# Performance work log

Hardware: AMD Instinct MI355X
Metric: run time of the kernel (lower is better)

## Reference

```python
import jax, jax.numpy as jnp
import numpy as np

# Static problem sizes (match input_specs): B graphs of NPG nodes each.
B = 64        # number of graphs in the batch
NPG = 1024    # nodes per graph
N = B * NPG   # total nodes
F = 64        # node feature dim
H = 128       # MLP hidden/output dim
K = 16        # knn neighbors (loop=False)


def setup_inputs() -> dict:
    key = jax.random.key(0)
    k1, k2, k3 = jax.random.split(key, 3)
    x = jax.random.normal(k1, (N, F), dtype=jnp.float32)
    batch = jnp.repeat(jnp.arange(B, dtype=jnp.int32), NPG)  # sorted graph ids
    W1 = jax.random.normal(k2, (2 * F, H), dtype=jnp.float32) / np.float32(np.sqrt(2 * F))
    b1 = jnp.zeros((H,), dtype=jnp.float32)
    W2 = jax.random.normal(k3, (H, H), dtype=jnp.float32) / np.float32(np.sqrt(H))
    b2 = jnp.zeros((H,), dtype=jnp.float32)
    return {"x": x, "batch": batch, "W1": W1, "b1": b1, "W2": W2, "b2": b2}


def _knn_edge_index(x):
    """PyG-style knn_graph (flow='source_to_target', loop=False) per graph.
    Returns (row, col) = edge_index[0], edge_index[1] where row = neighbor
    (source) node, col = center (target) node; each center has exactly K edges.
    Assumes batch ids are contiguous blocks of NPG nodes (as in setup_inputs)."""
    xb = x.reshape(B, NPG, F)
    sq = jnp.sum(xb * xb, axis=-1)                                   # [B, n]
    d = sq[:, :, None] + sq[:, None, :] - 2.0 * jnp.einsum('bnf,bmf->bnm', xb, xb)
    d = d + jnp.eye(NPG, dtype=d.dtype) * jnp.float32(1e10)          # no self loops
    _, nbr = jax.lax.top_k(-d, K)                                    # [B, n, K] local neighbor ids
    offs = (jnp.arange(B, dtype=jnp.int32) * NPG)[:, None, None]
    row = (nbr.astype(jnp.int32) + offs).reshape(-1)                 # neighbors (edge_index[0])
    centers = jnp.arange(N, dtype=jnp.int32).reshape(B, NPG, 1)
    col = jnp.broadcast_to(centers, (B, NPG, K)).reshape(-1)         # centers  (edge_index[1])
    return row, col


def reference(x, batch, W1, b1, W2, b2):
    # edge_index = knn_graph(x, k, batch, loop=False); row, col = edge_index
    row, col = _knn_edge_index(x)
    x_center = x[row]                                   # [E, F] gather
    x_neighbor = x[col]                                 # [E, F] gather
    ef = jnp.concatenate([x_center, x_neighbor - x_center], axis=-1)  # [E, 2F]
    # nn_module: Linear -> ReLU -> Linear -> ReLU
    h = jax.nn.relu(ef @ W1 + b1)
    h = jax.nn.relu(h @ W2 + b2)                        # [E, H]
    # manual scatter-mean onto row (index_add + bincount.clamp(min=1))
    node_features = jax.ops.segment_sum(h, row, num_segments=N)
    counts = jax.ops.segment_sum(jnp.ones((row.shape[0],), dtype=x.dtype), row, num_segments=N)
    counts = jnp.maximum(counts, 1.0)
    return node_features / counts[:, None]
```

## Files before the change

### kernel.cpp

```cpp
#include <hip/hip_runtime.h>

typedef __attribute__((ext_vector_type(4))) float f32x4;
typedef __attribute__((ext_vector_type(4))) unsigned int u32x4;
typedef __attribute__((ext_vector_type(8))) short s16x8;
typedef __attribute__((ext_vector_type(8))) _Float16 f16x8;

#define N_NODES 65536
#define GNPG 1024
#define FDIM 64
#define HDIM 128
#define KNN 16
#define JT 64
#define DSTR 68
#define SCAND 20
#define STKC 6
#define NEDGE (N_NODES * KNN)
#define NT (NEDGE / 64)

__global__ void prep_node_k(const float* __restrict__ x, float* __restrict__ sq,
                            double* __restrict__ sq64, _Float16* __restrict__ xf,
                            const float* __restrict__ W2, _Float16* __restrict__ w2f,
                            const float* __restrict__ W1, _Float16* __restrict__ w1cf) {
  if (blockIdx.x >= 1024) {
    int tid = threadIdx.x;
    if (blockIdx.x == 1024) {
      for (int idx = tid; idx < 8 * 4 * 64 * 8; idx += 256) {
        int j = idx & 7, l = (idx >> 3) & 63, ks = (idx >> 9) & 3, ct = idx >> 11;
        int k = 8 * (l >> 4) + j + 32 * ks, col = ct * 16 + (l & 15);
        w2f[idx] = (_Float16)W2[k * 128 + col];
      }
    } else {
      for (int idx = tid; idx < 16 * 2 * 64 * 8; idx += 256) {
        int j = idx & 7, l = (idx >> 3) & 63, ks = (idx >> 9) & 1, ct = idx >> 10;
        int k = 8 * (l >> 4) + j + 32 * ks, col = ct * 16 + (l & 15);
        float v = (col < 128) ? (W1[k * 128 + col] - W1[(k + 64) * 128 + col])
                              : W1[(k + 64) * 128 + (col - 128)];
        w1cf[idx] = (_Float16)v;
      }
    }
    return;
  }
  int t = blockIdx.x * 256 + threadIdx.x;
  int n = t >> 2, q = t & 3;
  const f32x4* xp = (const f32x4*)(x + (size_t)n * FDIM + q * 16);
  double s = 0;
  f16x8 h0, h1;
#pragma unroll
  for (int c8 = 0; c8 < 2; ++c8) {
    f32x4 a = xp[2 * c8], b = xp[2 * c8 + 1];
    f16x8 h;
#pragma unroll
    for (int e = 0; e < 4; ++e) {
      h[e] = (_Float16)a[e];
      h[4 + e] = (_Float16)b[e];
      s = fma((double)a[e], (double)a[e], s);
      s = fma((double)b[e], (double)b[e], s);
    }
    if (c8 == 0) h0 = h; else h1 = h;
  }
  *(f16x8*)(xf + (size_t)n * FDIM + q * 16) = h0;
  *(f16x8*)(xf + (size_t)n * FDIM + q * 16 + 8) = h1;
  s += __shfl_xor(s, 1);
  s += __shfl_xor(s, 2);
  if (q == 0) { sq64[n] = s; sq[n] = (float)s; }
}

__global__ __launch_bounds__(256) void prep_pq_k(const _Float16* __restrict__ xf,
                                                 const _Float16* __restrict__ w1cf,
                                                 const float* __restrict__ b1,
                                                 _Float16* __restrict__ PQ16) {
  __shared__ __attribute__((aligned(16))) _Float16 wcL[16384];
  int tid = threadIdx.x, lane = tid & 63, wave = tid >> 6;
  for (int i = tid; i < 2048; i += 256)
    *(f16x8*)(wcL + i * 8) = *(const f16x8*)(w1cf + i * 8);
  int rbase = blockIdx.x * 128 + wave * 32;
  f16x8 af[2][2];
#pragma unroll
  for (int rt = 0; rt < 2; ++rt)
#pragma unroll
    for (int ks = 0; ks < 2; ++ks) {
      size_t off = (size_t)(rbase + rt * 16 + (lane & 15)) * FDIM + (lane >> 4) * 8 + 32 * ks;
      af[rt][ks] = *(const f16x8*)(xf + off);
    }
  __syncthreads();
  f32x4 acc[2][16];
#pragma unroll
  for (int rt = 0; rt < 2; ++rt)
#pragma unroll
    for (int ct = 0; ct < 16; ++ct) acc[rt][ct] = (f32x4){0.f, 0.f, 0.f, 0.f};
#pragma unroll
  for (int ks = 0; ks < 2; ++ks)
#pragma unroll
    for (int ct = 0; ct < 16; ++ct) {
      f16x8 b = *(const f16x8*)(wcL + ((ct * 2 + ks) * 64 + lane) * 8);
#pragma unroll
      for (int rt = 0; rt < 2; ++rt)
        acc[rt][ct] = __builtin_amdgcn_mfma_f32_16x16x32_f16(af[rt][ks], b, acc[rt][ct], 0, 0, 0);
    }
  float b1r[16];
#pragma unroll
  for (int ct = 0; ct < 16; ++ct)
    b1r[ct] = (ct >= 8) ? b1[(ct - 8) * 16 + (lane & 15)] : 0.f;
#pragma unroll
  for (int rt = 0; rt < 2; ++rt)
#pragma unroll
    for (int ct = 0; ct < 16; ++ct) {
      int col = ct * 16 + (lane & 15);
#pragma unroll
      for (int r = 0; r < 4; ++r) {
        int row = rbase + rt * 16 + (lane >> 4) * 4 + r;
        PQ16[(size_t)row * 256 + col] = (_Float16)(acc[rt][ct][r] + b1r[ct]);
      }
    }
}

__global__ __launch_bounds__(256) void knn1_k(const _Float16* __restrict__ xf,
                                              const float* __restrict__ sq,
                                              unsigned short* __restrict__ candi) {
  __shared__ float sq_l[GNPG];
  __shared__ __attribute__((aligned(16))) _Float16 bfL[512 * 8];
  __shared__ __attribute__((aligned(16))) unsigned keyL[128 * DSTR];
  __shared__ __attribute__((aligned(16))) unsigned stk[STKC * 256];
  int tid = threadIdx.x, lane = tid & 63, wave = tid >> 6;
  int g = blockIdx.x >> 3;
  int rb = (blockIdx.x & 7) * 128;
  const _Float16* xfg = xf + (size_t)g * GNPG * FDIM;
  for (int i = tid; i < GNPG; i += 256) sq_l[i] = sq[g * GNPG + i] + 0.5f;
  f16x8 af[2][2];
#pragma unroll
  for (int rt = 0; rt < 2; ++rt)
#pragma unroll
    for (int ks = 0; ks < 2; ++ks) {
      size_t off = (size_t)(rb + wave * 32 + rt * 16 + (lane & 15)) * FDIM + (lane >> 4) * 8 + 32 * ks;
      af[rt][ks] = *(const f16x8*)(xfg + off);
    }
  unsigned dl[SCAND];
#pragma unroll
  for (int q = 0; q < SCAND; ++q) dl[q] = 0xFFFFFFFFu;
  int c = tid >> 1, sub = tid & 1;
  int sp = 0;
  for (int jt = 0; jt < GNPG / JT; ++jt) {
#pragma unroll
    for (int s2 = tid; s2 < 512; s2 += 256) {
      int ct = s2 >> 7, ks = (s2 >> 6) & 1, l = s2 & 63;
      size_t goff = (size_t)(jt * JT + ct * 16 + (l & 15)) * FDIM + (l >> 4) * 8 + 32 * ks;
      *(f16x8*)(bfL + s2 * 8) = *(const f16x8*)(xfg + goff);
    }
    __syncthreads();
    f32x4 acc[2][4];
#pragma unroll
    for (int rt = 0; rt < 2; ++rt)
#pragma unroll
      for (int ct = 0; ct < 4; ++ct) acc[rt][ct] = (f32x4){0.f, 0.f, 0.f, 0.f};
#pragma unroll
    for (int ks = 0; ks < 2; ++ks)
#pragma unroll
      for (int ct = 0; ct < 4; ++ct) {
        f16x8 bfr = *(const f16x8*)(bfL + ((ct * 2 + ks) * 64 + lane) * 8);
#pragma unroll
        for (int rt = 0; rt < 2; ++rt)
          acc[rt][ct] = __builtin_amdgcn_mfma_f32_16x16x32_f16(af[rt][ks], bfr, acc[rt][ct], 0, 0, 0);
      }
#pragma unroll
    for (int rt = 0; rt < 2; ++rt)
#pragma unroll
      for (int ct = 0; ct < 4; ++ct) {
        int coltl = ct * 16 + (lane & 15);
        int jlg = jt * JT + coltl;
        float sqj = sq_l[jlg];
#pragma unroll
        for (int r = 0; r < 4; ++r) {
          int row = wave * 32 + rt * 16 + (lane >> 4) * 4 + r;
          float d = sq_l[rb + row] + sqj - 2.f * acc[rt][ct][r];
          unsigned key = (__float_as_uint(d) & 0xFFFFFC00u) | (unsigned)jlg;
          if (rb + row == jlg) key = 0xFFFFFFFFu;
          keyL[row * DSTR + coltl] = key;
        }
      }
    __syncthreads();
    const unsigned* kp = keyL + c * DSTR + sub * 32;
    u32x4 vv[8];
#pragma unroll
    for (int i = 0; i < 8; ++i) vv[i] = *(const u32x4*)(kp + i * 4);
#pragma unroll
    for (int i = 0; i < 8; ++i) {
      if (__any(sp > STKC - 4)) {
        while (__any(sp > 0)) {
          if (sp > 0) {
            --sp;
            unsigned k = stk[sp * 256 + tid];
            if (k < dl[SCAND - 1]) {
              dl[SCAND - 1] = k;
#pragma unroll
              for (int p = SCAND - 1; p >= 1; --p) {
                unsigned mn = min(dl[p - 1], dl[p]);
                unsigned mx = max(dl[p - 1], dl[p]);
                dl[p - 1] = mn; dl[p] = mx;
              }
            }
          }
        }
      }
#pragma unroll
      for (int e = 0; e < 4; ++e) {
        stk[sp * 256 + tid] = vv[i][e];
        sp += (vv[i][e] < dl[SCAND - 1]) ? 1 : 0;
      }
    }
  }
  while (__any(sp > 0)) {
    if (sp > 0) {
      --sp;
      unsigned k = stk[sp * 256 + tid];
      if (k < dl[SCAND - 1]) {
        dl[SCAND - 1] = k;
#pragma unroll
        for (int p = SCAND - 1; p >= 1; --p) {
          unsigned mn = min(dl[p - 1], dl[p]);
          unsigned mx = max(dl[p - 1], dl[p]);
          dl[p - 1] = mn; dl[p] = mx;
        }
      }
    }
  }
  int nglob = g * GNPG + rb + c;
  unsigned short* ii = candi + (size_t)nglob * (2 * SCAND) + sub * SCAND;
#pragma unroll
  for (int q = 0; q < SCAND; ++q) ii[q] = (unsigned short)(dl[q] & 1023u);
}

__global__ __launch_bounds__(256) void knn2_k(const float* __restrict__ x,
                                              const double* __restrict__ sq64,
                                              const unsigned short* __restrict__ candi,
                                              int* __restrict__ nbr, int* __restrict__ counts) {
  __shared__ double md[2][128][17];
  __shared__ unsigned short mi[2][128][17];
  int tid = threadIdx.x, c_local = tid >> 1, sub = tid & 1;
  int n = blockIdx.x * 128 + c_local;
  int gbase = n & ~(GNPG - 1);
  f32x4 xi[16];
  const f32x4* xp = (const f32x4*)(x + (size_t)n * FDIM);
#pragma unroll
  for (int f = 0; f < 16; ++f) xi[f] = xp[f];
  double sq64i = sq64[n];
  double dl[KNN]; int il[KNN];
#pragma unroll
  for (int q = 0; q < KNN; ++q) { dl[q] = 1.0e300; il[q] = 0x7FFFFFFF; }
  const unsigned short* ii = candi + (size_t)n * (2 * SCAND) + sub * SCAND;
#pragma unroll 1
  for (int t = 0; t < SCAND; ++t) {
    int jl = ii[t];
    int j = gbase + jl;
    const f32x4* xj = (const f32x4*)(x + (size_t)j * FDIM);
    double t0 = 0, t1 = 0, t2 = 0, t3 = 0;
#pragma unroll
    for (int f = 0; f < 16; ++f) {
      f32x4 a = xi[f], b = xj[f];
      t0 = fma((double)a[0], (double)b[0], t0);
      t1 = fma((double)a[1], (double)b[1], t1);
      t2 = fma((double)a[2], (double)b[2], t2);
      t3 = fma((double)a[3], (double)b[3], t3);
    }
    double d = sq64i + sq64[j] - 2.0 * ((t0 + t1) + (t2 + t3));
    bool ins = (d < dl[KNN - 1]) || (d == dl[KNN - 1] && jl < il[KNN - 1]);
    if (ins) {
      dl[KNN - 1] = d; il[KNN - 1] = jl;
#pragma unroll
      for (int p = KNN - 1; p >= 1; --p) {
        double a0 = dl[p - 1], a1 = dl[p];
        int b0 = il[p - 1], b1v = il[p];
        bool cc = (a1 < a0) || (a1 == a0 && b1v < b0);
        dl[p - 1] = cc ? a1 : a0; dl[p] = cc ? a0 : a1;
        il[p - 1] = cc ? b1v : b0; il[p] = cc ? b0 : b1v;
      }
    }
  }
#pragma unroll
  for (int q = 0; q < KNN; ++q) {
    md[sub][c_local][q] = dl[q];
    mi[sub][c_local][q] = (unsigned short)il[q];
  }
  __syncthreads();
  if (sub == 0) {
    int pa = 0, pb = 0;
    for (int q = 0; q < KNN; ++q) {
      double da = md[0][c_local][pa]; int ia = mi[0][c_local][pa];
      double db = md[1][c_local][pb]; int ib = mi[1][c_local][pb];
      bool tb = (db < da) || (db == da && ib < ia);
      int iw = tb ? ib : ia;
      pa += !tb; pb += tb;
      int gidx = gbase + iw;
      nbr[(size_t)n * KNN + q] = gidx;
      atomicAdd(&counts[gidx], 1);
    }
  }
}

__global__ void scan_k(const int* __restrict__ counts, int* __restrict__ cursor) {
  __shared__ int wsum[16];
  int t = threadIdx.x;
  int base = t * 64;
  const int4* cp = (const int4*)(counts + base);
  int s = 0;
#pragma unroll
  for (int i = 0; i < 16; ++i) { int4 v = cp[i]; s += v.x + v.y + v.z + v.w; }
  int lane = t & 63, wv = t >> 6;
  int pre = s;
#pragma unroll
  for (int ofs = 1; ofs < 64; ofs <<= 1) {
    int o = __shfl_up(pre, ofs);
    if (lane >= ofs) pre += o;
  }
  if (lane == 63) wsum[wv] = pre;
  __syncthreads();
  if (t == 0) {
    int run = 0;
#pragma unroll
    for (int i = 0; i < 16; ++i) { int v = wsum[i]; wsum[i] = run; run += v; }
  }
  __syncthreads();
  int run = wsum[wv] + pre - s;
#pragma unroll
  for (int i = 0; i < 16; ++i) {
    int4 v = cp[i];
    cursor[base + 4 * i] = run; run += v.x;
    cursor[base + 4 * i + 1] = run; run += v.y;
    cursor[base + 4 * i + 2] = run; run += v.z;
    cursor[base + 4 * i + 3] = run; run += v.w;
  }
}

__global__ void scatter_k(const int* __restrict__ nbr, int* __restrict__ cursor,
                          int* __restrict__ srow, int* __restrict__ scol) {
  int e = blockIdx.x * 256 + threadIdx.x;
  int r = nbr[e], c = e >> 4;
  int pos = atomicAdd(&cursor[r], 1);
  srow[pos] = r; scol[pos] = c;
}

__global__ __launch_bounds__(256) void gemm2_k(const _Float16* __restrict__ PQ16,
                                               const int* __restrict__ srow, const int* __restrict__ scol,
                                               const _Float16* __restrict__ w2f,
                                               const float* __restrict__ b2,
                                               float* __restrict__ out) {
  __shared__ __attribute__((aligned(16))) char smem[16384];
  __shared__ int srowL[64];
  int tid = threadIdx.x, lane = tid & 63, wave = tid >> 6;
  int cg = wave & 1, eg = wave >> 1;
  f16x8 wf[4][4];
#pragma unroll
  for (int ct = 0; ct < 4; ++ct)
#pragma unroll
    for (int ks = 0; ks < 4; ++ks)
      wf[ct][ks] = *(const f16x8*)(w2f + ((((cg * 4 + ct) * 4 + ks) * 64 + lane) * 8));
  float b2r[4];
#pragma unroll
  for (int ct = 0; ct < 4; ++ct) b2r[ct] = b2[cg * 64 + ct * 16 + (lane & 15)];

  int e_in = tid >> 2, qq = tid & 3;
  f16x8 pf[8];
  int prow;
  {
    int e = blockIdx.x * 64 + e_in;
    prow = srow[e];
    int colc = scol[e];
    const f16x8* Pp = (const f16x8*)(PQ16 + (size_t)prow * 256 + qq * 32);
    const f16x8* Qp = (const f16x8*)(PQ16 + (size_t)colc * 256 + 128 + qq * 32);
#pragma unroll
    for (int i = 0; i < 4; ++i) { pf[i] = Pp[i]; pf[4 + i] = Qp[i]; }
  }
  for (int tile = blockIdx.x; tile < NT; tile += gridDim.x) {
    if (qq == 0) srowL[e_in] = prow;
#pragma unroll
    for (int i = 0; i < 4; ++i) {
      f16x8 hv;
#pragma unroll
      for (int e = 0; e < 8; ++e) {
        float sv = (float)pf[i][e] + (float)pf[4 + i][e];
        hv[e] = (_Float16)(sv > 0.f ? sv : 0.f);
      }
      int byteoff = e_in * 256 + ((2 * (qq * 32 + i * 8)) ^ ((e_in & 7) << 4));
      *(f16x8*)(smem + byteoff) = hv;
    }
    int ntile = tile + gridDim.x;
    if (ntile < NT) {
      int e = ntile * 64 + e_in;
      prow = srow[e];
      int colc = scol[e];
      const f16x8* Pp = (const f16x8*)(PQ16 + (size_t)prow * 256 + qq * 32);
      const f16x8* Qp = (const f16x8*)(PQ16 + (size_t)colc * 256 + 128 + qq * 32);
#pragma unroll
      for (int i = 0; i < 4; ++i) { pf[i] = Pp[i]; pf[4 + i] = Qp[i]; }
    }
    __syncthreads();
    f32x4 acc[2][4];
#pragma unroll
    for (int rt = 0; rt < 2; ++rt)
#pragma unroll
      for (int ct = 0; ct < 4; ++ct) acc[rt][ct] = (f32x4){0.f, 0.f, 0.f, 0.f};
#pragma unroll
    for (int rt = 0; rt < 2; ++rt) {
      int rowL = eg * 32 + rt * 16 + (lane & 15);
#pragma unroll
      for (int ks = 0; ks < 4; ++ks) {
        int byteoff = rowL * 256 + ((16 * (lane >> 4) + 64 * ks) ^ ((rowL & 7) << 4));
        f16x8 a = *(const f16x8*)(smem + byteoff);
#pragma unroll
        for (int ct = 0; ct < 4; ++ct)
          acc[rt][ct] = __builtin_amdgcn_mfma_f32_16x16x32_f16(a, wf[ct][ks], acc[rt][ct], 0, 0, 0);
      }
    }
    __syncthreads();
#pragma unroll
    for (int rt = 0; rt < 2; ++rt)
#pragma unroll
      for (int ct = 0; ct < 4; ++ct) {
        int col = cg * 64 + ct * 16 + (lane & 15);
#pragma unroll
        for (int r = 0; r < 4; ++r) {
          int row_in = eg * 32 + rt * 16 + (lane >> 4) * 4 + r;
          float v = acc[rt][ct][r] + b2r[ct];
          v = v > 0.f ? v : 0.f;
          int byteoff = row_in * 256 + ((2 * col) ^ ((row_in & 12) << 3));
          *(_Float16*)(smem + byteoff) = (_Float16)v;
        }
      }
    __syncthreads();
    {
      int col = tid & 127, estart = (tid >> 7) * 32;
      float a = 0.f;
      int prev = srowL[estart];
#pragma unroll 8
      for (int e2 = estart; e2 < estart + 32; ++e2) {
        int r2 = srowL[e2];
        if (r2 != prev) { atomicAdd(out + (size_t)prev * 128 + col, a); a = 0.f; prev = r2; }
        int byteoff = e2 * 256 + ((2 * col) ^ ((e2 & 12) << 3));
        a += (float)*(const _Float16*)(smem + byteoff);
      }
      atomicAdd(out + (size_t)prev * 128 + col, a);
    }
    __syncthreads();
  }
}

__global__ void final_k(float* __restrict__ out, const int* __restrict__ counts) {
  for (int i = blockIdx.x * 256 + threadIdx.x; i < N_NODES * 32; i += gridDim.x * 256) {
    f32x4 v = ((f32x4*)out)[i];
    int n = i >> 5;
    int c = counts[n];
    float inv = 1.0f / (float)(c > 0 ? c : 1);
    v[0] *= inv; v[1] *= inv; v[2] *= inv; v[3] *= inv;
    ((f32x4*)out)[i] = v;
  }
}

extern "C" void kernel_launch(void* const* d_in, const int* in_sizes, int n_in,
                              void* d_out, int out_size, void* d_ws, size_t ws_size,
                              hipStream_t stream) {
  const float* x = (const float*)d_in[0];
  const float* W1 = (const float*)d_in[2];
  const float* b1 = (const float*)d_in[3];
  const float* W2 = (const float*)d_in[4];
  const float* b2 = (const float*)d_in[5];
  float* out = (float*)d_out;
  char* ws = (char*)d_ws;

  _Float16* PQ16 = (_Float16*)(ws + 0);
  _Float16* xf = (_Float16*)(ws + 33554432);
  unsigned short* candi = (unsigned short*)(ws + 41943040);
  float* sq = (float*)(ws + 67108864);
  int* nbr = (int*)(ws + 67371008);
  int* counts = (int*)(ws + 71565312);
  int* cursor = (int*)(ws + 71827456);
  int* srow = (int*)(ws + 72089600);
  int* scol = (int*)(ws + 76283904);
  _Float16* w2f = (_Float16*)(ws + 80478208);
  _Float16* w1cf = (_Float16*)(ws + 80510976);
  double* sq64 = (double*)(ws + 80543744);

  hipMemsetAsync(d_out, 0, (size_t)out_size * sizeof(float), stream);
  hipMemsetAsync(counts, 0, (size_t)N_NODES * sizeof(int), stream);
  prep_node_k<<<1026, 256, 0, stream>>>(x, sq, sq64, xf, W2, w2f, W1, w1cf);
  knn1_k<<<N_NODES / 128, 256, 0, stream>>>(xf, sq, candi);
  knn2_k<<<N_NODES / 128, 256, 0, stream>>>(x, sq64, candi, nbr, counts);
  scan_k<<<1, 1024, 0, stream>>>(counts, cursor);
  scatter_k<<<NEDGE / 256, 256, 0, stream>>>(nbr, cursor, srow, scol);
  prep_pq_k<<<N_NODES / 128, 256, 0, stream>>>(xf, w1cf, b1, PQ16);
  gemm2_k<<<2048, 256, 0, stream>>>(PQ16, srow, scol, w2f, b2, out);
  final_k<<<2048, 256, 0, stream>>>(out, counts);
}
```

Measured before the change: 514.8 us.

## Split KNN candidate scan across four sub-threads per node with smaller row tiles

Each node's 1024-column candidate search in knn1 is now divided among four threads instead of two, with 64 rows per block and twice as many blocks. knn2 correspondingly refines 4x20 candidates per node and merges four sorted lists. This shortens the per-thread serial insertion work and raises parallelism. In exchange it halves MFMA row reuse of the loaded column tiles, doubles the fp64 refinement work and doubles candidate storage.

```diff
diff --git a/kernel.cpp b/kernel.cpp
--- a/kernel.cpp
+++ b/kernel.cpp
@@ -13,6 +13,7 @@
 #define JT 64
 #define DSTR 68
 #define SCAND 20
+#define NSUB 4
 #define STKC 6
 #define NEDGE (N_NODES * KNN)
 #define NT (NEDGE / 64)
@@ -119,25 +120,23 @@
                                               unsigned short* __restrict__ candi) {
   __shared__ float sq_l[GNPG];
   __shared__ __attribute__((aligned(16))) _Float16 bfL[512 * 8];
-  __shared__ __attribute__((aligned(16))) unsigned keyL[128 * DSTR];
+  __shared__ __attribute__((aligned(16))) unsigned keyL[64 * DSTR];
   __shared__ __attribute__((aligned(16))) unsigned stk[STKC * 256];
   int tid = threadIdx.x, lane = tid & 63, wave = tid >> 6;
-  int g = blockIdx.x >> 3;
-  int rb = (blockIdx.x & 7) * 128;
+  int g = blockIdx.x >> 4;
+  int rb = (blockIdx.x & 15) * 64;
   const _Float16* xfg = xf + (size_t)g * GNPG * FDIM;
   for (int i = tid; i < GNPG; i += 256) sq_l[i] = sq[g * GNPG + i] + 0.5f;
-  f16x8 af[2][2];
-#pragma unroll
-  for (int rt = 0; rt < 2; ++rt)
-#pragma unroll
-    for (int ks = 0; ks < 2; ++ks) {
-      size_t off = (size_t)(rb + wave * 32 + rt * 16 + (lane & 15)) * FDIM + (lane >> 4) * 8 + 32 * ks;
-      af[rt][ks] = *(const f16x8*)(xfg + off);
-    }
+  f16x8 af[2];
+#pragma unroll
+  for (int ks = 0; ks < 2; ++ks) {
+    size_t off = (size_t)(rb + wave * 16 + (lane & 15)) * FDIM + (lane >> 4) * 8 + 32 * ks;
+    af[ks] = *(const f16x8*)(xfg + off);
+  }
   unsigned dl[SCAND];
 #pragma unroll
   for (int q = 0; q < SCAND; ++q) dl[q] = 0xFFFFFFFFu;
-  int c = tid >> 1, sub = tid & 1;
+  int c = tid >> 2, sub = tid & 3;
   int sp = 0;
   for (int jt = 0; jt < GNPG / JT; ++jt) {
 #pragma unroll
@@ -147,43 +146,34 @@
       *(f16x8*)(bfL + s2 * 8) = *(const f16x8*)(xfg + goff);
     }
     __syncthreads();
-    f32x4 acc[2][4];
-#pragma unroll
-    for (int rt = 0; rt < 2; ++rt)
-#pragma unroll
-      for (int ct = 0; ct < 4; ++ct) acc[rt][ct] = (f32x4){0.f, 0.f, 0.f, 0.f};
+    f32x4 acc[4];
+#pragma unroll
+    for (int ct = 0; ct < 4; ++ct) acc[ct] = (f32x4){0.f, 0.f, 0.f, 0.f};
 #pragma unroll
     for (int ks = 0; ks < 2; ++ks)
 #pragma unroll
       for (int ct = 0; ct < 4; ++ct) {
         f16x8 bfr = *(const f16x8*)(bfL + ((ct * 2 + ks) * 64 + lane) * 8);
-#pragma unroll
-        for (int rt = 0; rt < 2; ++rt)
-          acc[rt][ct] = __builtin_amdgcn_mfma_f32_16x16x32_f16(af[rt][ks], bfr, acc[rt][ct], 0, 0, 0);
-      }
-#pragma unroll
-    for (int rt = 0; rt < 2; ++rt)
-#pragma unroll
-      for (int ct = 0; ct < 4; ++ct) {
-        int coltl = ct * 16 + (lane & 15);
-        int jlg = jt * JT + coltl;
-        float sqj = sq_l[jlg];
-#pragma unroll
-        for (int r = 0; r < 4; ++r) {
-          int row = wave * 32 + rt * 16 + (lane >> 4) * 4 + r;
-          float d = sq_l[rb + row] + sqj - 2.f * acc[rt][ct][r];
-          unsigned key = (__float_as_uint(d) & 0xFFFFFC00u) | (unsigned)jlg;
-          if (rb + row == jlg) key = 0xFFFFFFFFu;
-          keyL[row * DSTR + coltl] = key;
-        }
-      }
-    __syncthreads();
-    const unsigned* kp = keyL + c * DSTR + sub * 32;
-    u32x4 vv[8];
-#pragma unroll
-    for (int i = 0; i < 8; ++i) vv[i] = *(const u32x4*)(kp + i * 4);
-#pragma unroll
-    for (int i = 0; i < 8; ++i) {
+        acc[ct] = __builtin_amdgcn_mfma_f32_16x16x32_f16(af[ks], bfr, acc[ct], 0, 0, 0);
+      }
+#pragma unroll
+    for (int ct = 0; ct < 4; ++ct) {
+      int coltl = ct * 16 + (lane & 15);
+      int jlg = jt * JT + coltl;
+      float sqj = sq_l[jlg];
+#pragma unroll
+      for (int r = 0; r < 4; ++r) {
+        int row = wave * 16 + (lane >> 4) * 4 + r;
+        float d = sq_l[rb + row] + sqj - 2.f * acc[ct][r];
+        unsigned key = (__float_as_uint(d) & 0xFFFFFC00u) | (unsigned)jlg;
+        if (rb + row == jlg) key = 0xFFFFFFFFu;
+        keyL[row * DSTR + coltl] = key;
+      }
+    }
+    __syncthreads();
+    const unsigned* kp = keyL + c * DSTR + sub * 16;
+#pragma unroll 2
+    for (int i = 0; i < 4; ++i) {
       if (__any(sp > STKC - 4)) {
         while (__any(sp > 0)) {
           if (sp > 0) {
@@ -201,10 +191,11 @@
           }
         }
       }
+      u32x4 v = *(const u32x4*)(kp + i * 4);
 #pragma unroll
       for (int e = 0; e < 4; ++e) {
-        stk[sp * 256 + tid] = vv[i][e];
-        sp += (vv[i][e] < dl[SCAND - 1]) ? 1 : 0;
+        stk[sp * 256 + tid] = v[e];
+        sp += (v[e] < dl[SCAND - 1]) ? 1 : 0;
       }
     }
   }
@@ -224,7 +215,7 @@
     }
   }
   int nglob = g * GNPG + rb + c;
-  unsigned short* ii = candi + (size_t)nglob * (2 * SCAND) + sub * SCAND;
+  unsigned short* ii = candi + (size_t)nglob * (NSUB * SCAND) + sub * SCAND;
 #pragma unroll
   for (int q = 0; q < SCAND; ++q) ii[q] = (unsigned short)(dl[q] & 1023u);
 }
@@ -233,10 +224,10 @@
                                               const double* __restrict__ sq64,
                                               const unsigned short* __restrict__ candi,
                                               int* __restrict__ nbr, int* __restrict__ counts) {
-  __shared__ double md[2][128][17];
-  __shared__ unsigned short mi[2][128][17];
-  int tid = threadIdx.x, c_local = tid >> 1, sub = tid & 1;
-  int n = blockIdx.x * 128 + c_local;
+  __shared__ double md[NSUB][64][17];
+  __shared__ unsigned short mi[NSUB][64][17];
+  int tid = threadIdx.x, c_local = tid >> 2, sub = tid & 3;
+  int n = blockIdx.x * 64 + c_local;
   int gbase = n & ~(GNPG - 1);
   f32x4 xi[16];
   const f32x4* xp = (const f32x4*)(x + (size_t)n * FDIM);
@@ -246,7 +237,7 @@
   double dl[KNN]; int il[KNN];
 #pragma unroll
   for (int q = 0; q < KNN; ++q) { dl[q] = 1.0e300; il[q] = 0x7FFFFFFF; }
-  const unsigned short* ii = candi + (size_t)n * (2 * SCAND) + sub * SCAND;
+  const unsigned short* ii = candi + (size_t)n * (NSUB * SCAND) + sub * SCAND;
 #pragma unroll 1
   for (int t = 0; t < SCAND; ++t) {
     int jl = ii[t];
@@ -282,13 +273,19 @@
   }
   __syncthreads();
   if (sub == 0) {
-    int pa = 0, pb = 0;
+    int p0 = 0, p1 = 0, p2 = 0, p3 = 0;
     for (int q = 0; q < KNN; ++q) {
-      double da = md[0][c_local][pa]; int ia = mi[0][c_local][pa];
-      double db = md[1][c_local][pb]; int ib = mi[1][c_local][pb];
-      bool tb = (db < da) || (db == da && ib < ia);
-      int iw = tb ? ib : ia;
-      pa += !tb; pb += tb;
+      double h0 = md[0][c_local][p0]; int i0 = mi[0][c_local][p0];
+      double h1 = md[1][c_local][p1]; int i1 = mi[1][c_local][p1];
+      double h2 = md[2][c_local][p2]; int i2 = mi[2][c_local][p2];
+      double h3 = md[3][c_local][p3]; int i3 = mi[3][c_local][p3];
+      bool a01 = (h1 < h0) || (h1 == h0 && i1 < i0);
+      double ha = a01 ? h1 : h0; int ia = a01 ? i1 : i0; int wa = a01 ? 1 : 0;
+      bool a23 = (h3 < h2) || (h3 == h2 && i3 < i2);
+      double hb = a23 ? h3 : h2; int ib = a23 ? i3 : i2; int wb = a23 ? 3 : 2;
+      bool ab = (hb < ha) || (hb == ha && ib < ia);
+      int win = ab ? wb : wa; int iw = ab ? ib : ia;
+      p0 += (win == 0); p1 += (win == 1); p2 += (win == 2); p3 += (win == 3);
       int gidx = gbase + iw;
       nbr[(size_t)n * KNN + q] = gidx;
       atomicAdd(&counts[gidx], 1);
@@ -481,8 +478,8 @@
   hipMemsetAsync(d_out, 0, (size_t)out_size * sizeof(float), stream);
   hipMemsetAsync(counts, 0, (size_t)N_NODES * sizeof(int), stream);
   prep_node_k<<<1026, 256, 0, stream>>>(x, sq, sq64, xf, W2, w2f, W1, w1cf);
-  knn1_k<<<N_NODES / 128, 256, 0, stream>>>(xf, sq, candi);
-  knn2_k<<<N_NODES / 128, 256, 0, stream>>>(x, sq64, candi, nbr, counts);
+  knn1_k<<<N_NODES / 64, 256, 0, stream>>>(xf, sq, candi);
+  knn2_k<<<N_NODES / 64, 256, 0, stream>>>(x, sq64, candi, nbr, counts);
   scan_k<<<1, 1024, 0, stream>>>(counts, cursor);
   scatter_k<<<NEDGE / 256, 256, 0, stream>>>(nbr, cursor, srow, scol);
   prep_pq_k<<<N_NODES / 128, 256, 0, stream>>>(xf, w1cf, b1, PQ16);
```

Result: slower. 609.8 us (+18.4%).
